# Kernel tuning notes

Measured on AMD Instinct MI355X. Metric: run time of the kernel, lower is better.

The kernel has to match this reference:

```python
import jax, jax.numpy as jnp
import numpy as np

LAYERS = [256, 512, 512, 256]
DIM = 20
BATCH = 131072
PERIOD = 0.1
AMP = 1.0


def tri(x):
    # triangle wave centered around 0 with period PERIOD, amplitude AMP
    # matches: amplitude/period * (period - abs(x % (2p) - p) - p/2)
    return AMP / PERIOD * (PERIOD - jnp.abs(jnp.mod(x, 2.0 * PERIOD) - PERIOD) - PERIOD / 2.0)


def cdist(a, b):
    # pairwise euclidean distance between rows of a [m,d] and b [n,d] -> [m,n]
    d2 = (jnp.sum(a * a, axis=1)[:, None]
          + jnp.sum(b * b, axis=1)[None, :]
          - 2.0 * (a @ b.T))
    return jnp.sqrt(jnp.maximum(d2, 0.0))


def setup_inputs() -> dict:
    key = jax.random.key(0)
    ks = jax.random.split(key, 1 + len(LAYERS) + len(LAYERS))
    inp = {"x": jax.random.normal(ks[0], (BATCH, LAYERS[0]), dtype=jnp.float32)}
    # layer_params: uniform in [-1, 1), shape [l, DIM]
    for i, l in enumerate(LAYERS):
        inp[f"p{i}"] = jax.random.uniform(ks[1 + i], (l, DIM), dtype=jnp.float32,
                                          minval=-1.0, maxval=1.0)
    # layer_biases: uniform in [-0.1, 0.1), shape [l, 1]; only indices 1..n-1 are used
    for i in (1, 2, 3):
        inp[f"b{i}"] = jax.random.uniform(ks[1 + len(LAYERS) + i], (LAYERS[i], 1),
                                          dtype=jnp.float32, minval=-1.0, maxval=1.0) * 0.1
    return inp


def reference(x, p0, p1, p2, p3, b1, b2, b3):
    params = [p0, p1, p2, p3]
    biases = [None, b1, b2, b3]
    n = len(params)
    z = x
    for i in range(n - 1):
        l, lnext = params[i], params[i + 1]
        # synthesized weight: [l_i, l_{i+1}]
        W = tri(cdist(l, lnext)) / np.sqrt(l.shape[0]).astype(np.float32)
        z = z @ W + biases[i + 1].T  # bias [l_{i+1},1].T broadcasts over batch
        if i < n - 2:
            z = jax.nn.relu(z)
    return z
```

## Files before the change

kernel.cpp:

```cpp
#include <hip/hip_runtime.h>
#include <hip/hip_fp16.h>

typedef _Float16 f16x8 __attribute__((ext_vector_type(8)));
typedef _Float16 f16x4 __attribute__((ext_vector_type(4)));
typedef float    f32x4 __attribute__((ext_vector_type(4)));

#define BATCH 131072

__global__ void synth_weights_kernel(const float* __restrict__ p0, const float* __restrict__ p1,
                                     const float* __restrict__ p2, const float* __restrict__ p3,
                                     _Float16* __restrict__ blob0, _Float16* __restrict__ blob1,
                                     _Float16* __restrict__ blob2)
{
    const int idx = blockIdx.x * blockDim.x + threadIdx.x;
    const float* A; const float* B; _Float16* Wt; float scl; int e, n, k;
    if (idx < 131072) {
        A = p0; B = p1; Wt = blob0; scl = 0.0625f; e = idx;
        const int j = e & 7, lane = (e >> 3) & 63, t = e >> 9;
        const int ni = t & 3, pw = t >> 2, w = pw & 7, pid = pw >> 3;
        n = pid * 64 + ni * 16 + (lane & 15);
        k = w * 32 + ((lane >> 4) << 3) + j;
    } else if (idx < 393216) {
        A = p1; B = p2; Wt = blob1; scl = 0.04419417382415922f; e = idx - 131072;
        const int j = e & 7, lane = (e >> 3) & 63, t = e >> 9;
        const int ni = t & 3, pw = t >> 2, w = pw & 15, pid = pw >> 4;
        n = pid * 64 + ni * 16 + (lane & 15);
        k = w * 32 + ((lane >> 4) << 3) + j;
    } else {
        A = p2; B = p3; Wt = blob2; scl = 0.04419417382415922f; e = idx - 393216;
        const int j = e & 7, lane = (e >> 3) & 63, t = e >> 9;
        const int ni = t & 1, pw = t >> 1, w = pw & 15, pid = pw >> 4;
        n = pid * 32 + ni * 16 + (lane & 15);
        k = w * 32 + ((lane >> 4) << 3) + j;
    }
    float d2 = 0.f;
#pragma unroll
    for (int t = 0; t < 20; ++t) {
        float df = A[k * 20 + t] - B[n * 20 + t];
        d2 += df * df;
    }
    float d  = sqrtf(d2);
    float md = fmodf(d, 0.2f);
    float w  = 10.0f * (0.05f - fabsf(md - 0.1f)) * scl;
    Wt[(size_t)e] = (_Float16)w;
}

__device__ __forceinline__ f16x8 ld_act(const char* act, int mi, int rl, int hi, int w)
{
    const int row = mi * 16 + rl;
    const int c   = w * 4 + hi;
    return *(const f16x8*)(act + row * 1024 + ((c ^ (row & 7)) << 4));
}

template<int NW, int NI, int MI>
__device__ __forceinline__ void mm_reg(const char* act, const _Float16* __restrict__ blob,
                                       int lane, int pid, f32x4 (&acc)[NI][MI])
{
    const int rl = lane & 15;
    const int hi = lane >> 4;
    const char* wbase = (const char*)blob + ((size_t)pid * NW * NI) * 1024 + lane * 16;

    f16x8 wf[3][NI];
    f16x8 xfA[MI], xfB[MI];

#pragma unroll
    for (int ni = 0; ni < NI; ++ni) {
        wf[0][ni] = *(const f16x8*)(wbase + (0 * NI + ni) * 1024);
        wf[1][ni] = *(const f16x8*)(wbase + (1 * NI + ni) * 1024);
    }
#pragma unroll
    for (int mi = 0; mi < MI; ++mi) xfA[mi] = ld_act(act, mi, rl, hi, 0);

#pragma unroll
    for (int w = 0; w < NW; ++w) {
        if (w + 2 < NW) {
#pragma unroll
            for (int ni = 0; ni < NI; ++ni)
                wf[(w + 2) % 3][ni] = *(const f16x8*)(wbase + ((w + 2) * NI + ni) * 1024);
        }
        if (w + 1 < NW) {
            if ((w & 1) == 0) {
#pragma unroll
                for (int mi = 0; mi < MI; ++mi) xfB[mi] = ld_act(act, mi, rl, hi, w + 1);
            } else {
#pragma unroll
                for (int mi = 0; mi < MI; ++mi) xfA[mi] = ld_act(act, mi, rl, hi, w + 1);
            }
        }
        __builtin_amdgcn_s_setprio(1);
#pragma unroll
        for (int mi = 0; mi < MI; ++mi)
#pragma unroll
            for (int ni = 0; ni < NI; ++ni)
                acc[ni][mi] = __builtin_amdgcn_mfma_f32_16x16x32_f16(
                    wf[w % 3][ni], ((w & 1) == 0 ? xfA : xfB)[mi], acc[ni][mi], 0, 0, 0);
        __builtin_amdgcn_s_setprio(0);
    }
}

template<int NI, int MI>
__device__ __forceinline__ void store_z(char* act, const float* __restrict__ bias,
                                        int wc, int lane, f32x4 (&acc)[NI][MI])
{
    const int rl = lane & 15;
    const int hi = lane >> 4;
#pragma unroll
    for (int ni = 0; ni < NI; ++ni) {
        const int n0 = wc + ni * 16 + hi * 4;
        const float4 bv = *(const float4*)(bias + n0);
#pragma unroll
        for (int mi = 0; mi < MI; ++mi) {
            const int m = mi * 16 + rl;
            f16x4 h;
            h[0] = (_Float16)fmaxf(acc[ni][mi][0] + bv.x, 0.0f);
            h[1] = (_Float16)fmaxf(acc[ni][mi][1] + bv.y, 0.0f);
            h[2] = (_Float16)fmaxf(acc[ni][mi][2] + bv.z, 0.0f);
            h[3] = (_Float16)fmaxf(acc[ni][mi][3] + bv.w, 0.0f);
            *(f16x4*)(act + m * 1024 + (((n0 >> 3) ^ (m & 7)) << 4) + (n0 & 7) * 2) = h;
        }
    }
}

__global__ __launch_bounds__(512, 2)
void fused_mlp_kernel(const float* __restrict__ x,
                      const _Float16* __restrict__ blob0, const _Float16* __restrict__ blob1,
                      const _Float16* __restrict__ blob2,
                      const float* __restrict__ b1, const float* __restrict__ b2,
                      const float* __restrict__ b3,
                      float* __restrict__ out)
{
    extern __shared__ char act[];
    const int tid  = threadIdx.x;
    const int lane = tid & 63;
    const int wid  = tid >> 6;
    const size_t m0 = (size_t)blockIdx.x * 64;

#pragma unroll
    for (int it = 0; it < 4; ++it) {
        const int c   = it * 512 + tid;
        const int row = c >> 5;
        const int c8  = c & 31;
        const float* src = x + (m0 + row) * 256 + c8 * 8;
        const float4 v0 = *(const float4*)src;
        const float4 v1 = *(const float4*)(src + 4);
        f16x8 h;
        h[0] = (_Float16)v0.x; h[1] = (_Float16)v0.y; h[2] = (_Float16)v0.z; h[3] = (_Float16)v0.w;
        h[4] = (_Float16)v1.x; h[5] = (_Float16)v1.y; h[6] = (_Float16)v1.z; h[7] = (_Float16)v1.w;
        *(f16x8*)(act + row * 1024 + ((c8 ^ (row & 7)) << 4)) = h;
    }
    __syncthreads();

    const int wc = wid * 64;

    {
        f32x4 acc[4][4] = {};
        mm_reg<8, 4, 4>(act, blob0, lane, wid, acc);
        __syncthreads();
        store_z<4, 4>(act, b1, wc, lane, acc);
        __syncthreads();
    }

    {
        f32x4 acc[4][4] = {};
        mm_reg<16, 4, 4>(act, blob1, lane, wid, acc);
        __syncthreads();
        store_z<4, 4>(act, b2, wc, lane, acc);
        __syncthreads();
    }

    {
        const int wc3 = wid * 32;
        f32x4 acc[2][4] = {};
        mm_reg<16, 2, 4>(act, blob2, lane, wid, acc);

        const int rl = lane & 15;
        const int hi = lane >> 4;
        const float4 bv0 = *(const float4*)(b3 + wc3 + 0 * 16 + hi * 4);
        const float4 bv1 = *(const float4*)(b3 + wc3 + 1 * 16 + hi * 4);
#pragma unroll
        for (int mi = 0; mi < 4; ++mi) {
            const size_t m = m0 + mi * 16 + rl;
            f32x4 o0, o1;
            o0[0] = acc[0][mi][0] + bv0.x; o0[1] = acc[0][mi][1] + bv0.y;
            o0[2] = acc[0][mi][2] + bv0.z; o0[3] = acc[0][mi][3] + bv0.w;
            o1[0] = acc[1][mi][0] + bv1.x; o1[1] = acc[1][mi][1] + bv1.y;
            o1[2] = acc[1][mi][2] + bv1.z; o1[3] = acc[1][mi][3] + bv1.w;
            *(f32x4*)(out + m * 256 + wc3 + 0 * 16 + hi * 4) = o0;
            *(f32x4*)(out + m * 256 + wc3 + 1 * 16 + hi * 4) = o1;
        }
    }
}

extern "C" void kernel_launch(void* const* d_in, const int* in_sizes, int n_in,
                              void* d_out, int out_size, void* d_ws, size_t ws_size,
                              hipStream_t stream)
{
    const float* x  = (const float*)d_in[0];
    const float* p0 = (const float*)d_in[1];
    const float* p1 = (const float*)d_in[2];
    const float* p2 = (const float*)d_in[3];
    const float* p3 = (const float*)d_in[4];
    const float* b1 = (const float*)d_in[5];
    const float* b2 = (const float*)d_in[6];
    const float* b3 = (const float*)d_in[7];

    char* ws = (char*)d_ws;
    _Float16* blob0 = (_Float16*)(ws);
    _Float16* blob1 = (_Float16*)(ws + 262144);
    _Float16* blob2 = (_Float16*)(ws + 262144 + 524288);

    synth_weights_kernel<<<2048, 256, 0, stream>>>(p0, p1, p2, p3, blob0, blob1, blob2);

    fused_mlp_kernel<<<BATCH / 64, 512, 65536, stream>>>(x, blob0, blob1, blob2,
                                                         b1, b2, b3, (float*)d_out);
}
```

Measured before the change: 174.8 us.

## Switch MLP matmuls to 32x32x16 MFMA with matching weight layout

```diff
diff --git a/kernel.cpp b/kernel.cpp
--- a/kernel.cpp
+++ b/kernel.cpp
@@ -1,9 +1,10 @@
 #include <hip/hip_runtime.h>
 #include <hip/hip_fp16.h>
 
-typedef _Float16 f16x8 __attribute__((ext_vector_type(8)));
-typedef _Float16 f16x4 __attribute__((ext_vector_type(4)));
-typedef float    f32x4 __attribute__((ext_vector_type(4)));
+typedef _Float16 f16x8  __attribute__((ext_vector_type(8)));
+typedef _Float16 f16x4  __attribute__((ext_vector_type(4)));
+typedef float    f32x4  __attribute__((ext_vector_type(4)));
+typedef float    f32x16 __attribute__((ext_vector_type(16)));
 
 #define BATCH 131072
 
@@ -17,21 +18,21 @@
     if (idx < 131072) {
         A = p0; B = p1; Wt = blob0; scl = 0.0625f; e = idx;
         const int j = e & 7, lane = (e >> 3) & 63, t = e >> 9;
-        const int ni = t & 3, pw = t >> 2, w = pw & 7, pid = pw >> 3;
-        n = pid * 64 + ni * 16 + (lane & 15);
-        k = w * 32 + ((lane >> 4) << 3) + j;
+        const int ni2 = t & 1, pw = t >> 1, w = pw & 15, pid = pw >> 4;
+        n = pid * 64 + ni2 * 32 + (lane & 31);
+        k = w * 16 + ((lane >> 5) << 3) + j;
     } else if (idx < 393216) {
         A = p1; B = p2; Wt = blob1; scl = 0.04419417382415922f; e = idx - 131072;
         const int j = e & 7, lane = (e >> 3) & 63, t = e >> 9;
-        const int ni = t & 3, pw = t >> 2, w = pw & 15, pid = pw >> 4;
-        n = pid * 64 + ni * 16 + (lane & 15);
-        k = w * 32 + ((lane >> 4) << 3) + j;
+        const int ni2 = t & 1, pw = t >> 1, w = pw & 31, pid = pw >> 5;
+        n = pid * 64 + ni2 * 32 + (lane & 31);
+        k = w * 16 + ((lane >> 5) << 3) + j;
     } else {
         A = p2; B = p3; Wt = blob2; scl = 0.04419417382415922f; e = idx - 393216;
         const int j = e & 7, lane = (e >> 3) & 63, t = e >> 9;
-        const int ni = t & 1, pw = t >> 1, w = pw & 15, pid = pw >> 4;
-        n = pid * 32 + ni * 16 + (lane & 15);
-        k = w * 32 + ((lane >> 4) << 3) + j;
+        const int w = t & 31, pid = t >> 5;
+        n = pid * 32 + (lane & 31);
+        k = w * 16 + ((lane >> 5) << 3) + j;
     }
     float d2 = 0.f;
 #pragma unroll
@@ -45,83 +46,86 @@
     Wt[(size_t)e] = (_Float16)w;
 }
 
-__device__ __forceinline__ f16x8 ld_act(const char* act, int mi, int rl, int hi, int w)
-{
-    const int row = mi * 16 + rl;
-    const int c   = w * 4 + hi;
+__device__ __forceinline__ f16x8 ld_act32(const char* act, int mi2, int rl32, int hi2, int w)
+{
+    const int row = mi2 * 32 + rl32;
+    const int c   = w * 2 + hi2;
     return *(const f16x8*)(act + row * 1024 + ((c ^ (row & 7)) << 4));
 }
 
-template<int NW, int NI, int MI>
-__device__ __forceinline__ void mm_reg(const char* act, const _Float16* __restrict__ blob,
-                                       int lane, int pid, f32x4 (&acc)[NI][MI])
-{
-    const int rl = lane & 15;
-    const int hi = lane >> 4;
-    const char* wbase = (const char*)blob + ((size_t)pid * NW * NI) * 1024 + lane * 16;
-
-    f16x8 wf[3][NI];
-    f16x8 xfA[MI], xfB[MI];
-
-#pragma unroll
-    for (int ni = 0; ni < NI; ++ni) {
-        wf[0][ni] = *(const f16x8*)(wbase + (0 * NI + ni) * 1024);
-        wf[1][ni] = *(const f16x8*)(wbase + (1 * NI + ni) * 1024);
-    }
-#pragma unroll
-    for (int mi = 0; mi < MI; ++mi) xfA[mi] = ld_act(act, mi, rl, hi, 0);
+template<int NW, int NI2, int MI2>
+__device__ __forceinline__ void mm32(const char* act, const _Float16* __restrict__ blob,
+                                     int lane, int pid, f32x16 (&acc)[NI2][MI2])
+{
+    const int rl32 = lane & 31;
+    const int hi2  = lane >> 5;
+    const char* wbase = (const char*)blob + ((size_t)pid * NW * NI2) * 1024 + lane * 16;
+
+    f16x8 wf[3][NI2];
+    f16x8 xfA[MI2], xfB[MI2];
+
+#pragma unroll
+    for (int ni = 0; ni < NI2; ++ni) {
+        wf[0][ni] = *(const f16x8*)(wbase + (0 * NI2 + ni) * 1024);
+        wf[1][ni] = *(const f16x8*)(wbase + (1 * NI2 + ni) * 1024);
+    }
+#pragma unroll
+    for (int mi = 0; mi < MI2; ++mi) xfA[mi] = ld_act32(act, mi, rl32, hi2, 0);
 
 #pragma unroll
     for (int w = 0; w < NW; ++w) {
         if (w + 2 < NW) {
 #pragma unroll
-            for (int ni = 0; ni < NI; ++ni)
-                wf[(w + 2) % 3][ni] = *(const f16x8*)(wbase + ((w + 2) * NI + ni) * 1024);
+            for (int ni = 0; ni < NI2; ++ni)
+                wf[(w + 2) % 3][ni] = *(const f16x8*)(wbase + ((w + 2) * NI2 + ni) * 1024);
         }
         if (w + 1 < NW) {
             if ((w & 1) == 0) {
 #pragma unroll
-                for (int mi = 0; mi < MI; ++mi) xfB[mi] = ld_act(act, mi, rl, hi, w + 1);
+                for (int mi = 0; mi < MI2; ++mi) xfB[mi] = ld_act32(act, mi, rl32, hi2, w + 1);
             } else {
 #pragma unroll
-                for (int mi = 0; mi < MI; ++mi) xfA[mi] = ld_act(act, mi, rl, hi, w + 1);
+                for (int mi = 0; mi < MI2; ++mi) xfA[mi] = ld_act32(act, mi, rl32, hi2, w + 1);
             }
         }
         __builtin_amdgcn_s_setprio(1);
 #pragma unroll
-        for (int mi = 0; mi < MI; ++mi)
-#pragma unroll
-            for (int ni = 0; ni < NI; ++ni)
-                acc[ni][mi] = __builtin_amdgcn_mfma_f32_16x16x32_f16(
+        for (int mi = 0; mi < MI2; ++mi)
+#pragma unroll
+            for (int ni = 0; ni < NI2; ++ni)
+                acc[ni][mi] = __builtin_amdgcn_mfma_f32_32x32x16_f16(
                     wf[w % 3][ni], ((w & 1) == 0 ? xfA : xfB)[mi], acc[ni][mi], 0, 0, 0);
         __builtin_amdgcn_s_setprio(0);
     }
 }
 
-template<int NI, int MI>
-__device__ __forceinline__ void store_z(char* act, const float* __restrict__ bias,
-                                        int wc, int lane, f32x4 (&acc)[NI][MI])
-{
-    const int rl = lane & 15;
-    const int hi = lane >> 4;
-#pragma unroll
-    for (int ni = 0; ni < NI; ++ni) {
-        const int n0 = wc + ni * 16 + hi * 4;
-        const float4 bv = *(const float4*)(bias + n0);
-#pragma unroll
-        for (int mi = 0; mi < MI; ++mi) {
-            const int m = mi * 16 + rl;
-            f16x4 h;
-            h[0] = (_Float16)fmaxf(acc[ni][mi][0] + bv.x, 0.0f);
-            h[1] = (_Float16)fmaxf(acc[ni][mi][1] + bv.y, 0.0f);
-            h[2] = (_Float16)fmaxf(acc[ni][mi][2] + bv.z, 0.0f);
-            h[3] = (_Float16)fmaxf(acc[ni][mi][3] + bv.w, 0.0f);
-            *(f16x4*)(act + m * 1024 + (((n0 >> 3) ^ (m & 7)) << 4) + (n0 & 7) * 2) = h;
-        }
-    }
-}
-
-__global__ __launch_bounds__(512, 2)
+template<int NI2, int MI2>
+__device__ __forceinline__ void store_z32(char* act, const float* __restrict__ bias,
+                                          int wc, int lane, f32x16 (&acc)[NI2][MI2])
+{
+    const int rl32 = lane & 31;
+    const int hi2  = lane >> 5;
+#pragma unroll
+    for (int ni = 0; ni < NI2; ++ni) {
+#pragma unroll
+        for (int mi = 0; mi < MI2; ++mi) {
+            const int m = mi * 32 + rl32;
+#pragma unroll
+            for (int g = 0; g < 4; ++g) {
+                const int n0 = wc + ni * 32 + g * 8 + hi2 * 4;
+                const float4 bv = *(const float4*)(bias + n0);
+                f16x4 h;
+                h[0] = (_Float16)fmaxf(acc[ni][mi][g * 4 + 0] + bv.x, 0.0f);
+                h[1] = (_Float16)fmaxf(acc[ni][mi][g * 4 + 1] + bv.y, 0.0f);
+                h[2] = (_Float16)fmaxf(acc[ni][mi][g * 4 + 2] + bv.z, 0.0f);
+                h[3] = (_Float16)fmaxf(acc[ni][mi][g * 4 + 3] + bv.w, 0.0f);
+                *(f16x4*)(act + m * 1024 + (((n0 >> 3) ^ (m & 7)) << 4) + (n0 & 7) * 2) = h;
+            }
+        }
+    }
+}
+
+__global__ __launch_bounds__(512, 4)
 void fused_mlp_kernel(const float* __restrict__ x,
                       const _Float16* __restrict__ blob0, const _Float16* __restrict__ blob1,
                       const _Float16* __restrict__ blob2,
@@ -153,40 +157,42 @@
     const int wc = wid * 64;
 
     {
-        f32x4 acc[4][4] = {};
-        mm_reg<8, 4, 4>(act, blob0, lane, wid, acc);
-        __syncthreads();
-        store_z<4, 4>(act, b1, wc, lane, acc);
+        f32x16 acc[2][2] = {};
+        mm32<16, 2, 2>(act, blob0, lane, wid, acc);
+        __syncthreads();
+        store_z32<2, 2>(act, b1, wc, lane, acc);
         __syncthreads();
     }
 
     {
-        f32x4 acc[4][4] = {};
-        mm_reg<16, 4, 4>(act, blob1, lane, wid, acc);
-        __syncthreads();
-        store_z<4, 4>(act, b2, wc, lane, acc);
+        f32x16 acc[2][2] = {};
+        mm32<32, 2, 2>(act, blob1, lane, wid, acc);
+        __syncthreads();
+        store_z32<2, 2>(act, b2, wc, lane, acc);
         __syncthreads();
     }
 
     {
         const int wc3 = wid * 32;
-        f32x4 acc[2][4] = {};
-        mm_reg<16, 2, 4>(act, blob2, lane, wid, acc);
-
-        const int rl = lane & 15;
-        const int hi = lane >> 4;
-        const float4 bv0 = *(const float4*)(b3 + wc3 + 0 * 16 + hi * 4);
-        const float4 bv1 = *(const float4*)(b3 + wc3 + 1 * 16 + hi * 4);
-#pragma unroll
-        for (int mi = 0; mi < 4; ++mi) {
-            const size_t m = m0 + mi * 16 + rl;
-            f32x4 o0, o1;
-            o0[0] = acc[0][mi][0] + bv0.x; o0[1] = acc[0][mi][1] + bv0.y;
-            o0[2] = acc[0][mi][2] + bv0.z; o0[3] = acc[0][mi][3] + bv0.w;
-            o1[0] = acc[1][mi][0] + bv1.x; o1[1] = acc[1][mi][1] + bv1.y;
-            o1[2] = acc[1][mi][2] + bv1.z; o1[3] = acc[1][mi][3] + bv1.w;
-            *(f32x4*)(out + m * 256 + wc3 + 0 * 16 + hi * 4) = o0;
-            *(f32x4*)(out + m * 256 + wc3 + 1 * 16 + hi * 4) = o1;
+        f32x16 acc[1][2] = {};
+        mm32<32, 1, 2>(act, blob2, lane, wid, acc);
+
+        const int rl32 = lane & 31;
+        const int hi2  = lane >> 5;
+#pragma unroll
+        for (int mi = 0; mi < 2; ++mi) {
+            const size_t m = m0 + mi * 32 + rl32;
+#pragma unroll
+            for (int g = 0; g < 4; ++g) {
+                const int n0 = wc3 + g * 8 + hi2 * 4;
+                const float4 bv = *(const float4*)(b3 + n0);
+                f32x4 o;
+                o[0] = acc[0][mi][g * 4 + 0] + bv.x;
+                o[1] = acc[0][mi][g * 4 + 1] + bv.y;
+                o[2] = acc[0][mi][g * 4 + 2] + bv.z;
+                o[3] = acc[0][mi][g * 4 + 3] + bv.w;
+                *(f32x4*)(out + m * 256 + n0) = o;
+            }
         }
     }
 }
```

Result: slower. 272.8 us (+56.0%).
